# Kernel tuning notes

Measured on AMD Instinct MI355X. Metric: run time of the kernel, lower is better.

## Reference

```python
import jax, jax.numpy as jnp
import numpy as np

N_NODES = 8192
N_EDGES = 262144
IN_DIM = 128
HID = 256


def _sage_conv(x, src, dst, w_l, b_l, w_r, n):
    # PyG SAGEConv: out = lin_l(mean_{j in N(i)} x_j) + lin_r(x_i)
    agg = jax.ops.segment_sum(x[src], dst, num_segments=n)          # [n, d]
    deg = jax.ops.segment_sum(jnp.ones_like(src, dtype=x.dtype), dst, num_segments=n)
    mean = agg / jnp.maximum(deg, 1.0)[:, None]
    return mean @ w_l.T + b_l + x @ w_r.T


def setup_inputs() -> dict:
    key = jax.random.key(0)
    ks = jax.random.split(key, 12)
    s = lambda d: 1.0 / np.sqrt(d)
    x = jax.random.normal(ks[0], (N_NODES, IN_DIM), dtype=jnp.float32)
    edge_index = jax.random.randint(ks[1], (2, N_EDGES), 0, N_NODES, dtype=jnp.int64)
    return {
        "x": x,
        "edge_index": edge_index,
        "wl1": jax.random.uniform(ks[2], (HID, IN_DIM), jnp.float32, -s(IN_DIM), s(IN_DIM)),
        "bl1": jax.random.uniform(ks[3], (HID,), jnp.float32, -s(IN_DIM), s(IN_DIM)),
        "wr1": jax.random.uniform(ks[4], (HID, IN_DIM), jnp.float32, -s(IN_DIM), s(IN_DIM)),
        "wl2": jax.random.uniform(ks[5], (HID, HID), jnp.float32, -s(HID), s(HID)),
        "bl2": jax.random.uniform(ks[6], (HID,), jnp.float32, -s(HID), s(HID)),
        "wr2": jax.random.uniform(ks[7], (HID, HID), jnp.float32, -s(HID), s(HID)),
        "w_out": jax.random.uniform(ks[8], (HID, HID), jnp.float32, -s(HID), s(HID)),
        "b_out": jax.random.uniform(ks[9], (HID,), jnp.float32, -s(HID), s(HID)),
        "w_edge": jax.random.uniform(ks[10], (1, 2 * HID), jnp.float32, -s(2 * HID), s(2 * HID)),
        "b_edge": jax.random.uniform(ks[11], (1,), jnp.float32, -s(2 * HID), s(2 * HID)),
    }


def reference(x, edge_index, wl1, bl1, wr1, wl2, bl2, wr2, w_out, b_out, w_edge, b_edge):
    n = x.shape[0]
    src, dst = edge_index[0], edge_index[1]
    h = jax.nn.relu(_sage_conv(x, src, dst, wl1, bl1, wr1, n))
    h = jax.nn.relu(_sage_conv(h, src, dst, wl2, bl2, wr2, n))
    h = h @ w_out.T + b_out                                          # [n, HID]
    # edge_logits[i, j] = edge_proj(cat(h_i, h_j)) == <w_left, h_i> + <w_right, h_j> + b
    w_left, w_right = w_edge[0, :HID], w_edge[0, HID:]
    li = h @ w_left                                                  # [n]
    lj = h @ w_right                                                 # [n]
    return li[:, None] + lj[None, :] + b_edge[0]                     # [n, n]
```

## Files before the change

### kernel.cpp

```cpp
#include <hip/hip_runtime.h>

#define NN   8192
#define NE   262144
#define IND  128
#define HIDD 256

typedef __bf16 v8bf __attribute__((ext_vector_type(8)));
typedef float  v4f  __attribute__((ext_vector_type(4)));

__device__ __forceinline__ float bf2f(unsigned short u) {
  unsigned int v = ((unsigned int)u) << 16;
  return __builtin_bit_cast(float, v);
}
__device__ __forceinline__ unsigned short f2bf(float f) {
  unsigned int u = __builtin_bit_cast(unsigned int, f);
  u += 0x7FFF + ((u >> 16) & 1);
  return (unsigned short)(u >> 16);
}

__global__ void k_buildW1(const float* __restrict__ wl1,
                          const float* __restrict__ wr1,
                          unsigned short* __restrict__ W1) {
  int t = blockIdx.x * 256 + threadIdx.x;
  int n = t >> 8, k = t & 255;
  float v = (k < 128) ? wl1[n * 128 + k] : wr1[n * 128 + (k - 128)];
  W1[t] = f2bf(v);
}
__global__ void k_buildW2(const float* __restrict__ wl2,
                          const float* __restrict__ wr2,
                          unsigned short* __restrict__ W2) {
  int t = blockIdx.x * 256 + threadIdx.x;
  int n = t >> 9, k = t & 511;
  float v = (k < 256) ? wl2[n * 256 + k] : wr2[n * 256 + (k - 256)];
  W2[t] = f2bf(v);
}
__global__ void k_vlr(const float* __restrict__ w_out,
                      const float* __restrict__ b_out,
                      const float* __restrict__ w_edge,
                      float* __restrict__ vl, float* __restrict__ vr,
                      float* __restrict__ c2) {
  int k = threadIdx.x;
  float al = 0.f, ar = 0.f;
  for (int n = 0; n < 256; n++) {
    float w = w_out[n * 256 + k];
    al += w * w_edge[n];
    ar += w * w_edge[256 + n];
  }
  vl[k] = al; vr[k] = ar;
  __shared__ float red[256];
  red[k] = b_out[k] * w_edge[k];
  __syncthreads();
  for (int s = 128; s > 0; s >>= 1) { if (k < s) red[k] += red[k + s]; __syncthreads(); }
  if (k == 0) c2[0] = red[0];
  __syncthreads();
  red[k] = b_out[k] * w_edge[256 + k];
  __syncthreads();
  for (int s = 128; s > 0; s >>= 1) { if (k < s) red[k] += red[k + s]; __syncthreads(); }
  if (k == 0) c2[1] = red[0];
}

__global__ void k_count(const int* __restrict__ dst, int* __restrict__ counts) {
  int e = blockIdx.x * 256 + threadIdx.x;
  if (e < NE) atomicAdd(&counts[dst[e]], 1);
}
__global__ void k_scan(const int* __restrict__ counts, int* __restrict__ offs,
                       int* __restrict__ curs, float* __restrict__ ideg) {
  __shared__ int sums[256];
  int t = threadIdx.x;
  int base = t * 32;
  int s = 0;
  for (int i = 0; i < 32; i++) s += counts[base + i];
  sums[t] = s;
  __syncthreads();
  for (int off = 1; off < 256; off <<= 1) {
    int v = (t >= off) ? sums[t - off] : 0;
    __syncthreads();
    sums[t] += v;
    __syncthreads();
  }
  int run = (t == 0) ? 0 : sums[t - 1];
  for (int i = 0; i < 32; i++) {
    int c = counts[base + i];
    offs[base + i] = run;
    curs[base + i] = run;
    ideg[base + i] = 1.0f / (float)(c > 0 ? c : 1);
    run += c;
  }
}
__global__ void k_fill(const int* __restrict__ src, const int* __restrict__ dst,
                       int* __restrict__ curs, int* __restrict__ csr) {
  int e = blockIdx.x * 256 + threadIdx.x;
  if (e < NE) {
    int d = dst[e];
    int p = atomicAdd(&curs[d], 1);
    csr[p] = src[e];
  }
}

__global__ void k_copyx(const float* __restrict__ x, unsigned short* __restrict__ A1) {
  int t = blockIdx.x * 256 + threadIdx.x;
  int row = t >> 4, c8 = (t & 15) << 3;
  const float* xp = &x[row * 128 + c8];
  float4 a = *(const float4*)xp;
  float4 b = *(const float4*)(xp + 4);
  unsigned short o[8];
  o[0] = f2bf(a.x); o[1] = f2bf(a.y); o[2] = f2bf(a.z); o[3] = f2bf(a.w);
  o[4] = f2bf(b.x); o[5] = f2bf(b.y); o[6] = f2bf(b.z); o[7] = f2bf(b.w);
  *(uint4*)&A1[row * 256 + 128 + c8] = *(uint4*)o;
}

__global__ void k_gather_f32(const float* __restrict__ feat,
                             unsigned short* __restrict__ outp,
                             const int* __restrict__ offs, const int* __restrict__ counts,
                             const float* __restrict__ ideg, const int* __restrict__ csr) {
  int node = blockIdx.x;
  int t = threadIdx.x;
  int start = offs[node], cnt = counts[node];
  const float* fp = feat + t;
  float acc = 0.f;
  int i = 0;
  for (; i + 4 <= cnt; i += 4) {
    int s0 = csr[start + i], s1 = csr[start + i + 1];
    int s2 = csr[start + i + 2], s3 = csr[start + i + 3];
    acc += fp[(size_t)s0 * IND];
    acc += fp[(size_t)s1 * IND];
    acc += fp[(size_t)s2 * IND];
    acc += fp[(size_t)s3 * IND];
  }
  for (; i < cnt; i++) acc += fp[(size_t)csr[start + i] * IND];
  outp[(size_t)node * 256 + t] = f2bf(acc * ideg[node]);
}

__global__ void k_gather_bf16(const unsigned short* __restrict__ feat, int fstride, int foff,
                              unsigned short* __restrict__ outp, int ostride, int ooff,
                              const int* __restrict__ offs, const int* __restrict__ counts,
                              const float* __restrict__ ideg, const int* __restrict__ csr) {
  int node = blockIdx.x;
  int t = threadIdx.x;
  int start = offs[node], cnt = counts[node];
  const unsigned short* fp = feat + foff + t;
  float acc = 0.f;
  int i = 0;
  for (; i + 4 <= cnt; i += 4) {
    int s0 = csr[start + i], s1 = csr[start + i + 1];
    int s2 = csr[start + i + 2], s3 = csr[start + i + 3];
    acc += bf2f(fp[(size_t)s0 * fstride]);
    acc += bf2f(fp[(size_t)s1 * fstride]);
    acc += bf2f(fp[(size_t)s2 * fstride]);
    acc += bf2f(fp[(size_t)s3 * fstride]);
  }
  for (; i < cnt; i++) acc += bf2f(fp[(size_t)csr[start + i] * fstride]);
  outp[(size_t)node * ostride + ooff + t] = f2bf(acc * ideg[node]);
}

__global__ __launch_bounds__(256) void k_gemm(
    const unsigned short* __restrict__ A, int lda,
    const unsigned short* __restrict__ B,
    const float* __restrict__ bias,
    unsigned short* __restrict__ C, int ldc, int coff, int K) {
  __shared__ __align__(16) unsigned short As[64][40];
  __shared__ __align__(16) unsigned short Bs[64][40];
  int tid = threadIdx.x;
  int bm = blockIdx.x, bn = blockIdx.y;
  int lane = tid & 63, wave = tid >> 6;
  int wm = (wave & 1) * 32, wn = (wave >> 1) * 32;
  int quad = lane >> 4, l16 = lane & 15;
  int srow = tid >> 2, schunk = (tid & 3) * 8;
  const unsigned short* gA = A + (size_t)(bm * 64 + srow) * lda + schunk;
  const unsigned short* gB = B + (size_t)(bn * 64 + srow) * K + schunk;
  v4f acc[2][2];
  for (int mi = 0; mi < 2; mi++)
    for (int ni = 0; ni < 2; ni++)
      acc[mi][ni] = v4f{0.f, 0.f, 0.f, 0.f};
  for (int k0 = 0; k0 < K; k0 += 32) {
    uint4 va = *(const uint4*)(gA + k0);
    uint4 vb = *(const uint4*)(gB + k0);
    __syncthreads();
    *(uint4*)&As[srow][schunk] = va;
    *(uint4*)&Bs[srow][schunk] = vb;
    __syncthreads();
    v8bf a0 = *(v8bf*)&As[wm + l16][quad * 8];
    v8bf a1 = *(v8bf*)&As[wm + 16 + l16][quad * 8];
    v8bf b0 = *(v8bf*)&Bs[wn + l16][quad * 8];
    v8bf b1 = *(v8bf*)&Bs[wn + 16 + l16][quad * 8];
    acc[0][0] = __builtin_amdgcn_mfma_f32_16x16x32_bf16(a0, b0, acc[0][0], 0, 0, 0);
    acc[0][1] = __builtin_amdgcn_mfma_f32_16x16x32_bf16(a0, b1, acc[0][1], 0, 0, 0);
    acc[1][0] = __builtin_amdgcn_mfma_f32_16x16x32_bf16(a1, b0, acc[1][0], 0, 0, 0);
    acc[1][1] = __builtin_amdgcn_mfma_f32_16x16x32_bf16(a1, b1, acc[1][1], 0, 0, 0);
  }
  for (int mi = 0; mi < 2; mi++) {
    for (int ni = 0; ni < 2; ni++) {
      int col = bn * 64 + wn + ni * 16 + l16;
      float bv = bias[col];
      for (int r = 0; r < 4; r++) {
        int row = bm * 64 + wm + mi * 16 + quad * 4 + r;
        float v = acc[mi][ni][r] + bv;
        v = fmaxf(v, 0.f);
        C[(size_t)row * ldc + coff + col] = f2bf(v);
      }
    }
  }
}

__global__ void k_lilj(const unsigned short* __restrict__ H2,
                       const float* __restrict__ vl, const float* __restrict__ vr,
                       const float* __restrict__ c2, const float* __restrict__ b_edge,
                       float* __restrict__ Li, float* __restrict__ Lj) {
  int wave = threadIdx.x >> 6, lane = threadIdx.x & 63;
  int node = blockIdx.x * 4 + wave;
  const unsigned short* h = H2 + (size_t)node * 256;
  float al = 0.f, ar = 0.f;
  for (int k = lane; k < 256; k += 64) {
    float hv = bf2f(h[k]);
    al += hv * vl[k];
    ar += hv * vr[k];
  }
  for (int off = 32; off > 0; off >>= 1) {
    al += __shfl_down(al, off);
    ar += __shfl_down(ar, off);
  }
  if (lane == 0) {
    Li[node] = al + c2[0] + b_edge[0];
    Lj[node] = ar + c2[1];
  }
}

__global__ void k_outer(const float* __restrict__ Li, const float* __restrict__ Lj,
                        float* __restrict__ outp) {
  int t = blockIdx.x * 256 + threadIdx.x;
  int row = t >> 10;
  int jc = (t & 1023) << 3;
  float li = Li[row];
  float4 x0 = *(const float4*)&Lj[jc];
  float4 x1 = *(const float4*)&Lj[jc + 4];
  float4 o0, o1;
  o0.x = li + x0.x; o0.y = li + x0.y; o0.z = li + x0.z; o0.w = li + x0.w;
  o1.x = li + x1.x; o1.y = li + x1.y; o1.z = li + x1.z; o1.w = li + x1.w;
  float* op = &outp[(size_t)row * 8192 + jc];
  *(float4*)op = o0;
  *(float4*)(op + 4) = o1;
}

extern "C" void kernel_launch(void* const* d_in, const int* in_sizes, int n_in,
                              void* d_out, int out_size, void* d_ws, size_t ws_size,
                              hipStream_t stream) {
  const float* x      = (const float*)d_in[0];
  const int*   ei     = (const int*)d_in[1];
  const float* wl1    = (const float*)d_in[2];
  const float* bl1    = (const float*)d_in[3];
  const float* wr1    = (const float*)d_in[4];
  const float* wl2    = (const float*)d_in[5];
  const float* bl2    = (const float*)d_in[6];
  const float* wr2    = (const float*)d_in[7];
  const float* w_out  = (const float*)d_in[8];
  const float* b_out  = (const float*)d_in[9];
  const float* w_edge = (const float*)d_in[10];
  const float* b_edge = (const float*)d_in[11];
  float* outp = (float*)d_out;

  const int* srcp = ei;
  const int* dstp = ei + NE;

  const size_t OFF_A1   = 0;
  const size_t OFF_A2   = OFF_A1 + 4194304;
  const size_t OFF_H2   = OFF_A2 + 8388608;
  const size_t OFF_W1   = OFF_H2 + 4194304;
  const size_t OFF_W2   = OFF_W1 + 131072;
  const size_t OFF_VL   = OFF_W2 + 262144;
  const size_t OFF_VR   = OFF_VL + 1024;
  const size_t OFF_C2   = OFF_VR + 1024;
  const size_t OFF_CNT  = OFF_C2 + 256;
  const size_t OFF_OFFS = OFF_CNT + 32768;
  const size_t OFF_CURS = OFF_OFFS + 32768;
  const size_t OFF_IDEG = OFF_CURS + 32768;
  const size_t OFF_CSR  = OFF_IDEG + 32768;
  const size_t OFF_LI   = OFF_CSR + 1048576;
  const size_t OFF_LJ   = OFF_LI + 32768;
  const size_t TOTAL    = OFF_LJ + 32768;
  if (ws_size < TOTAL) return;

  char* ws = (char*)d_ws;
  unsigned short* A1 = (unsigned short*)(ws + OFF_A1);
  unsigned short* A2 = (unsigned short*)(ws + OFF_A2);
  unsigned short* H2 = (unsigned short*)(ws + OFF_H2);
  unsigned short* W1 = (unsigned short*)(ws + OFF_W1);
  unsigned short* W2 = (unsigned short*)(ws + OFF_W2);
  float* VL   = (float*)(ws + OFF_VL);
  float* VR   = (float*)(ws + OFF_VR);
  float* C2   = (float*)(ws + OFF_C2);
  int*   CNT  = (int*)(ws + OFF_CNT);
  int*   OFFS = (int*)(ws + OFF_OFFS);
  int*   CURS = (int*)(ws + OFF_CURS);
  float* IDEG = (float*)(ws + OFF_IDEG);
  int*   CSR  = (int*)(ws + OFF_CSR);
  float* LI   = (float*)(ws + OFF_LI);
  float* LJ   = (float*)(ws + OFF_LJ);

  hipMemsetAsync(CNT, 0, NN * sizeof(int), stream);

  k_buildW1<<<256, 256, 0, stream>>>(wl1, wr1, W1);
  k_buildW2<<<512, 256, 0, stream>>>(wl2, wr2, W2);
  k_vlr<<<1, 256, 0, stream>>>(w_out, b_out, w_edge, VL, VR, C2);
  k_copyx<<<512, 256, 0, stream>>>(x, A1);

  k_count<<<NE / 256, 256, 0, stream>>>(dstp, CNT);
  k_scan<<<1, 256, 0, stream>>>(CNT, OFFS, CURS, IDEG);
  k_fill<<<NE / 256, 256, 0, stream>>>(srcp, dstp, CURS, CSR);

  k_gather_f32<<<NN, 128, 0, stream>>>(x, A1, OFFS, CNT, IDEG, CSR);
  k_gemm<<<dim3(NN / 64, 4), 256, 0, stream>>>(A1, 256, W1, bl1, A2, 512, 256, 256);

  k_gather_bf16<<<NN, 256, 0, stream>>>(A2, 512, 256, A2, 512, 0, OFFS, CNT, IDEG, CSR);
  k_gemm<<<dim3(NN / 64, 4), 256, 0, stream>>>(A2, 512, W2, bl2, H2, 256, 0, 512);

  k_lilj<<<NN / 4, 256, 0, stream>>>(H2, VL, VR, C2, b_edge, LI, LJ);
  k_outer<<<(NN * 1024) / 256, 256, 0, stream>>>(LI, LJ, outp);
}
```

Before: 425.1 us.

## Fuse prep kernels, wave-per-node vectorized gathers, fuse GEMM2 with logit projection

Merges the weight packing, x conversion, counter zeroing and vl/vr computation into one multi-role launch. Rewrites both neighbour gathers to use one wave per node with vectorized loads and several accumulators. Fuses the second GEMM epilogue with the li/lj dot products via shuffle reductions and atomics, which removes the H2 buffer and the k_lilj pass. The outer-sum kernel now uses nontemporal stores and folds the constants in. The risks are float atomic ordering nondeterminism and contention on the LI/LJ atomics.

```diff
diff --git a/kernel.cpp b/kernel.cpp
--- a/kernel.cpp
+++ b/kernel.cpp
@@ -18,45 +18,66 @@
   return (unsigned short)(u >> 16);
 }
 
-__global__ void k_buildW1(const float* __restrict__ wl1,
-                          const float* __restrict__ wr1,
-                          unsigned short* __restrict__ W1) {
-  int t = blockIdx.x * 256 + threadIdx.x;
-  int n = t >> 8, k = t & 255;
-  float v = (k < 128) ? wl1[n * 128 + k] : wr1[n * 128 + (k - 128)];
-  W1[t] = f2bf(v);
-}
-__global__ void k_buildW2(const float* __restrict__ wl2,
-                          const float* __restrict__ wr2,
-                          unsigned short* __restrict__ W2) {
-  int t = blockIdx.x * 256 + threadIdx.x;
-  int n = t >> 9, k = t & 511;
-  float v = (k < 256) ? wl2[n * 256 + k] : wr2[n * 256 + (k - 256)];
-  W2[t] = f2bf(v);
-}
-__global__ void k_vlr(const float* __restrict__ w_out,
-                      const float* __restrict__ b_out,
-                      const float* __restrict__ w_edge,
-                      float* __restrict__ vl, float* __restrict__ vr,
-                      float* __restrict__ c2) {
-  int k = threadIdx.x;
-  float al = 0.f, ar = 0.f;
-  for (int n = 0; n < 256; n++) {
-    float w = w_out[n * 256 + k];
-    al += w * w_edge[n];
-    ar += w * w_edge[256 + n];
-  }
-  vl[k] = al; vr[k] = ar;
+__global__ void k_prep(const float* __restrict__ wl1, const float* __restrict__ wr1,
+                       const float* __restrict__ wl2, const float* __restrict__ wr2,
+                       const float* __restrict__ x,
+                       const float* __restrict__ w_out, const float* __restrict__ b_out,
+                       const float* __restrict__ w_edge,
+                       unsigned short* __restrict__ W1, unsigned short* __restrict__ W2,
+                       unsigned short* __restrict__ A1,
+                       float* __restrict__ VL, float* __restrict__ VR,
+                       float* __restrict__ C2,
+                       int* __restrict__ CNT,
+                       float* __restrict__ LI, float* __restrict__ LJ) {
   __shared__ float red[256];
-  red[k] = b_out[k] * w_edge[k];
-  __syncthreads();
-  for (int s = 128; s > 0; s >>= 1) { if (k < s) red[k] += red[k + s]; __syncthreads(); }
-  if (k == 0) c2[0] = red[0];
-  __syncthreads();
-  red[k] = b_out[k] * w_edge[256 + k];
-  __syncthreads();
-  for (int s = 128; s > 0; s >>= 1) { if (k < s) red[k] += red[k + s]; __syncthreads(); }
-  if (k == 0) c2[1] = red[0];
+  int b = blockIdx.x, tid = threadIdx.x;
+  if (b < 256) {
+    int t = b * 256 + tid;
+    int n = t >> 8, k = t & 255;
+    float v = (k < 128) ? wl1[n * 128 + k] : wr1[n * 128 + (k - 128)];
+    W1[t] = f2bf(v);
+  } else if (b < 768) {
+    int t = (b - 256) * 256 + tid;
+    int n = t >> 9, k = t & 511;
+    float v = (k < 256) ? wl2[n * 256 + k] : wr2[n * 256 + (k - 256)];
+    W2[t] = f2bf(v);
+  } else if (b < 1280) {
+    int t = (b - 768) * 256 + tid;
+    int row = t >> 4, c8 = (t & 15) << 3;
+    const float* xp = &x[row * 128 + c8];
+    float4 a = *(const float4*)xp;
+    float4 bb = *(const float4*)(xp + 4);
+    unsigned short o[8];
+    o[0] = f2bf(a.x);  o[1] = f2bf(a.y);  o[2] = f2bf(a.z);  o[3] = f2bf(a.w);
+    o[4] = f2bf(bb.x); o[5] = f2bf(bb.y); o[6] = f2bf(bb.z); o[7] = f2bf(bb.w);
+    *(uint4*)&A1[row * 256 + 128 + c8] = *(uint4*)o;
+  } else if (b < 1312) {
+    CNT[(b - 1280) * 256 + tid] = 0;
+  } else if (b < 1344) {
+    int t = (b - 1312) * 256 + tid;
+    LI[t] = 0.f; LJ[t] = 0.f;
+  } else {
+    int k = tid;
+    float al = 0.f, ar = 0.f;
+    for (int n = 0; n < 256; n += 8) {
+#pragma unroll
+      for (int u = 0; u < 8; u++) {
+        float w = w_out[(n + u) * 256 + k];
+        al = fmaf(w, w_edge[n + u], al);
+        ar = fmaf(w, w_edge[256 + n + u], ar);
+      }
+    }
+    VL[k] = al; VR[k] = ar;
+    red[k] = b_out[k] * w_edge[k];
+    __syncthreads();
+    for (int s = 128; s > 0; s >>= 1) { if (k < s) red[k] += red[k + s]; __syncthreads(); }
+    if (k == 0) C2[0] = red[0];
+    __syncthreads();
+    red[k] = b_out[k] * w_edge[256 + k];
+    __syncthreads();
+    for (int s = 128; s > 0; s >>= 1) { if (k < s) red[k] += red[k + s]; __syncthreads(); }
+    if (k == 0) C2[1] = red[0];
+  }
 }
 
 __global__ void k_count(const int* __restrict__ dst, int* __restrict__ counts) {
@@ -68,8 +89,12 @@
   __shared__ int sums[256];
   int t = threadIdx.x;
   int base = t * 32;
+  int c[32];
+#pragma unroll
+  for (int i = 0; i < 32; i += 4) *(int4*)&c[i] = *(const int4*)&counts[base + i];
   int s = 0;
-  for (int i = 0; i < 32; i++) s += counts[base + i];
+#pragma unroll
+  for (int i = 0; i < 32; i++) s += c[i];
   sums[t] = s;
   __syncthreads();
   for (int off = 1; off < 256; off <<= 1) {
@@ -79,12 +104,12 @@
     __syncthreads();
   }
   int run = (t == 0) ? 0 : sums[t - 1];
+#pragma unroll
   for (int i = 0; i < 32; i++) {
-    int c = counts[base + i];
     offs[base + i] = run;
     curs[base + i] = run;
-    ideg[base + i] = 1.0f / (float)(c > 0 ? c : 1);
-    run += c;
+    ideg[base + i] = 1.0f / (float)(c[i] > 0 ? c[i] : 1);
+    run += c[i];
   }
 }
 __global__ void k_fill(const int* __restrict__ src, const int* __restrict__ dst,
@@ -97,60 +122,72 @@
   }
 }
 
-__global__ void k_copyx(const float* __restrict__ x, unsigned short* __restrict__ A1) {
-  int t = blockIdx.x * 256 + threadIdx.x;
-  int row = t >> 4, c8 = (t & 15) << 3;
-  const float* xp = &x[row * 128 + c8];
-  float4 a = *(const float4*)xp;
-  float4 b = *(const float4*)(xp + 4);
-  unsigned short o[8];
-  o[0] = f2bf(a.x); o[1] = f2bf(a.y); o[2] = f2bf(a.z); o[3] = f2bf(a.w);
-  o[4] = f2bf(b.x); o[5] = f2bf(b.y); o[6] = f2bf(b.z); o[7] = f2bf(b.w);
-  *(uint4*)&A1[row * 256 + 128 + c8] = *(uint4*)o;
-}
-
-__global__ void k_gather_f32(const float* __restrict__ feat,
-                             unsigned short* __restrict__ outp,
-                             const int* __restrict__ offs, const int* __restrict__ counts,
-                             const float* __restrict__ ideg, const int* __restrict__ csr) {
-  int node = blockIdx.x;
-  int t = threadIdx.x;
+__global__ void k_gather1(const float* __restrict__ x, unsigned short* __restrict__ A1,
+                          const int* __restrict__ offs, const int* __restrict__ counts,
+                          const float* __restrict__ ideg, const int* __restrict__ csr) {
+  int lane = threadIdx.x & 63;
+  int node = blockIdx.x * 4 + (threadIdx.x >> 6);
   int start = offs[node], cnt = counts[node];
-  const float* fp = feat + t;
-  float acc = 0.f;
+  const float2* fp = (const float2*)x + lane;
+  float ax0 = 0.f, ay0 = 0.f, ax1 = 0.f, ay1 = 0.f;
+  int i = 0;
+  for (; i + 8 <= cnt; i += 8) {
+    int s0 = csr[start + i + 0], s1 = csr[start + i + 1];
+    int s2 = csr[start + i + 2], s3 = csr[start + i + 3];
+    int s4 = csr[start + i + 4], s5 = csr[start + i + 5];
+    int s6 = csr[start + i + 6], s7 = csr[start + i + 7];
+    float2 v0 = fp[(size_t)s0 * 64], v1 = fp[(size_t)s1 * 64];
+    float2 v2 = fp[(size_t)s2 * 64], v3 = fp[(size_t)s3 * 64];
+    float2 v4 = fp[(size_t)s4 * 64], v5 = fp[(size_t)s5 * 64];
+    float2 v6 = fp[(size_t)s6 * 64], v7 = fp[(size_t)s7 * 64];
+    ax0 += v0.x; ay0 += v0.y; ax0 += v1.x; ay0 += v1.y;
+    ax0 += v2.x; ay0 += v2.y; ax0 += v3.x; ay0 += v3.y;
+    ax1 += v4.x; ay1 += v4.y; ax1 += v5.x; ay1 += v5.y;
+    ax1 += v6.x; ay1 += v6.y; ax1 += v7.x; ay1 += v7.y;
+  }
+  for (; i < cnt; i++) {
+    float2 v = fp[(size_t)csr[start + i] * 64];
+    ax0 += v.x; ay0 += v.y;
+  }
+  float sc = ideg[node];
+  float mx = (ax0 + ax1) * sc, my = (ay0 + ay1) * sc;
+  unsigned int o = (unsigned int)f2bf(mx) | ((unsigned int)f2bf(my) << 16);
+  *(unsigned int*)&A1[(size_t)node * 256 + lane * 2] = o;
+}
+
+__global__ void k_gather2(const unsigned short* __restrict__ A2,
+                          unsigned short* __restrict__ A2w,
+                          const int* __restrict__ offs, const int* __restrict__ counts,
+                          const float* __restrict__ ideg, const int* __restrict__ csr) {
+  int lane = threadIdx.x & 63;
+  int node = blockIdx.x * 4 + (threadIdx.x >> 6);
+  int start = offs[node], cnt = counts[node];
+  const unsigned short* fp = A2 + 256 + lane * 4;
+  float a0 = 0.f, a1 = 0.f, a2 = 0.f, a3 = 0.f;
+#define ACC4(v) { a0 += bf2f((unsigned short)((v).x));        \
+                  a1 += bf2f((unsigned short)((v).x >> 16));  \
+                  a2 += bf2f((unsigned short)((v).y));        \
+                  a3 += bf2f((unsigned short)((v).y >> 16)); }
   int i = 0;
   for (; i + 4 <= cnt; i += 4) {
-    int s0 = csr[start + i], s1 = csr[start + i + 1];
+    int s0 = csr[start + i + 0], s1 = csr[start + i + 1];
     int s2 = csr[start + i + 2], s3 = csr[start + i + 3];
-    acc += fp[(size_t)s0 * IND];
-    acc += fp[(size_t)s1 * IND];
-    acc += fp[(size_t)s2 * IND];
-    acc += fp[(size_t)s3 * IND];
-  }
-  for (; i < cnt; i++) acc += fp[(size_t)csr[start + i] * IND];
-  outp[(size_t)node * 256 + t] = f2bf(acc * ideg[node]);
-}
-
-__global__ void k_gather_bf16(const unsigned short* __restrict__ feat, int fstride, int foff,
-                              unsigned short* __restrict__ outp, int ostride, int ooff,
-                              const int* __restrict__ offs, const int* __restrict__ counts,
-                              const float* __restrict__ ideg, const int* __restrict__ csr) {
-  int node = blockIdx.x;
-  int t = threadIdx.x;
-  int start = offs[node], cnt = counts[node];
-  const unsigned short* fp = feat + foff + t;
-  float acc = 0.f;
-  int i = 0;
-  for (; i + 4 <= cnt; i += 4) {
-    int s0 = csr[start + i], s1 = csr[start + i + 1];
-    int s2 = csr[start + i + 2], s3 = csr[start + i + 3];
-    acc += bf2f(fp[(size_t)s0 * fstride]);
-    acc += bf2f(fp[(size_t)s1 * fstride]);
-    acc += bf2f(fp[(size_t)s2 * fstride]);
-    acc += bf2f(fp[(size_t)s3 * fstride]);
-  }
-  for (; i < cnt; i++) acc += bf2f(fp[(size_t)csr[start + i] * fstride]);
-  outp[(size_t)node * ostride + ooff + t] = f2bf(acc * ideg[node]);
+    uint2 v0 = *(const uint2*)&fp[(size_t)s0 * 512];
+    uint2 v1 = *(const uint2*)&fp[(size_t)s1 * 512];
+    uint2 v2 = *(const uint2*)&fp[(size_t)s2 * 512];
+    uint2 v3 = *(const uint2*)&fp[(size_t)s3 * 512];
+    ACC4(v0); ACC4(v1); ACC4(v2); ACC4(v3);
+  }
+  for (; i < cnt; i++) {
+    uint2 v = *(const uint2*)&fp[(size_t)csr[start + i] * 512];
+    ACC4(v);
+  }
+#undef ACC4
+  float sc = ideg[node];
+  unsigned int lo = (unsigned int)f2bf(a0 * sc) | ((unsigned int)f2bf(a1 * sc) << 16);
+  unsigned int hi = (unsigned int)f2bf(a2 * sc) | ((unsigned int)f2bf(a3 * sc) << 16);
+  uint2 o; o.x = lo; o.y = hi;
+  *(uint2*)&A2w[(size_t)node * 512 + lane * 4] = o;
 }
 
 __global__ __launch_bounds__(256) void k_gemm(
@@ -202,43 +239,93 @@
   }
 }
 
-__global__ void k_lilj(const unsigned short* __restrict__ H2,
-                       const float* __restrict__ vl, const float* __restrict__ vr,
-                       const float* __restrict__ c2, const float* __restrict__ b_edge,
-                       float* __restrict__ Li, float* __restrict__ Lj) {
-  int wave = threadIdx.x >> 6, lane = threadIdx.x & 63;
-  int node = blockIdx.x * 4 + wave;
-  const unsigned short* h = H2 + (size_t)node * 256;
-  float al = 0.f, ar = 0.f;
-  for (int k = lane; k < 256; k += 64) {
-    float hv = bf2f(h[k]);
-    al += hv * vl[k];
-    ar += hv * vr[k];
-  }
-  for (int off = 32; off > 0; off >>= 1) {
-    al += __shfl_down(al, off);
-    ar += __shfl_down(ar, off);
-  }
-  if (lane == 0) {
-    Li[node] = al + c2[0] + b_edge[0];
-    Lj[node] = ar + c2[1];
+__global__ __launch_bounds__(256) void k_gemm2_lilj(
+    const unsigned short* __restrict__ A,
+    const unsigned short* __restrict__ B,
+    const float* __restrict__ bias,
+    const float* __restrict__ VL, const float* __restrict__ VR,
+    float* __restrict__ LI, float* __restrict__ LJ) {
+  __shared__ __align__(16) unsigned short As[64][40];
+  __shared__ __align__(16) unsigned short Bs[64][40];
+  int tid = threadIdx.x;
+  int bm = blockIdx.x, bn = blockIdx.y;
+  int lane = tid & 63, wave = tid >> 6;
+  int wm = (wave & 1) * 32, wn = (wave >> 1) * 32;
+  int quad = lane >> 4, l16 = lane & 15;
+  int srow = tid >> 2, schunk = (tid & 3) * 8;
+  const unsigned short* gA = A + (size_t)(bm * 64 + srow) * 512 + schunk;
+  const unsigned short* gB = B + (size_t)(bn * 64 + srow) * 512 + schunk;
+  v4f acc[2][2];
+  for (int mi = 0; mi < 2; mi++)
+    for (int ni = 0; ni < 2; ni++)
+      acc[mi][ni] = v4f{0.f, 0.f, 0.f, 0.f};
+  for (int k0 = 0; k0 < 512; k0 += 32) {
+    uint4 va = *(const uint4*)(gA + k0);
+    uint4 vb = *(const uint4*)(gB + k0);
+    __syncthreads();
+    *(uint4*)&As[srow][schunk] = va;
+    *(uint4*)&Bs[srow][schunk] = vb;
+    __syncthreads();
+    v8bf a0 = *(v8bf*)&As[wm + l16][quad * 8];
+    v8bf a1 = *(v8bf*)&As[wm + 16 + l16][quad * 8];
+    v8bf b0 = *(v8bf*)&Bs[wn + l16][quad * 8];
+    v8bf b1 = *(v8bf*)&Bs[wn + 16 + l16][quad * 8];
+    acc[0][0] = __builtin_amdgcn_mfma_f32_16x16x32_bf16(a0, b0, acc[0][0], 0, 0, 0);
+    acc[0][1] = __builtin_amdgcn_mfma_f32_16x16x32_bf16(a0, b1, acc[0][1], 0, 0, 0);
+    acc[1][0] = __builtin_amdgcn_mfma_f32_16x16x32_bf16(a1, b0, acc[1][0], 0, 0, 0);
+    acc[1][1] = __builtin_amdgcn_mfma_f32_16x16x32_bf16(a1, b1, acc[1][1], 0, 0, 0);
+  }
+  int colb = bn * 64 + wn + l16;
+  float vl0 = VL[colb], vl1 = VL[colb + 16];
+  float vr0 = VR[colb], vr1 = VR[colb + 16];
+  float bv0 = bias[colb], bv1 = bias[colb + 16];
+  float pli[8], plj[8];
+#pragma unroll
+  for (int mi = 0; mi < 2; mi++) {
+#pragma unroll
+    for (int r = 0; r < 4; r++) {
+      float v0 = fmaxf(acc[mi][0][r] + bv0, 0.f);
+      float v1 = fmaxf(acc[mi][1][r] + bv1, 0.f);
+      pli[mi * 4 + r] = v0 * vl0 + v1 * vl1;
+      plj[mi * 4 + r] = v0 * vr0 + v1 * vr1;
+    }
+  }
+#pragma unroll
+  for (int off = 1; off < 16; off <<= 1) {
+#pragma unroll
+    for (int idx = 0; idx < 8; idx++) {
+      pli[idx] += __shfl_xor(pli[idx], off);
+      plj[idx] += __shfl_xor(plj[idx], off);
+    }
+  }
+  if (l16 == 0) {
+#pragma unroll
+    for (int mi = 0; mi < 2; mi++) {
+#pragma unroll
+      for (int r = 0; r < 4; r++) {
+        int row = bm * 64 + wm + mi * 16 + quad * 4 + r;
+        atomicAdd(&LI[row], pli[mi * 4 + r]);
+        atomicAdd(&LJ[row], plj[mi * 4 + r]);
+      }
+    }
   }
 }
 
 __global__ void k_outer(const float* __restrict__ Li, const float* __restrict__ Lj,
+                        const float* __restrict__ C2, const float* __restrict__ b_edge,
                         float* __restrict__ outp) {
   int t = blockIdx.x * 256 + threadIdx.x;
   int row = t >> 10;
   int jc = (t & 1023) << 3;
-  float li = Li[row];
-  float4 x0 = *(const float4*)&Lj[jc];
-  float4 x1 = *(const float4*)&Lj[jc + 4];
-  float4 o0, o1;
-  o0.x = li + x0.x; o0.y = li + x0.y; o0.z = li + x0.z; o0.w = li + x0.w;
-  o1.x = li + x1.x; o1.y = li + x1.y; o1.z = li + x1.z; o1.w = li + x1.w;
+  float cst = C2[0] + C2[1] + b_edge[0];
+  float li = Li[row] + cst;
+  v4f x0 = *(const v4f*)&Lj[jc];
+  v4f x1 = *(const v4f*)&Lj[jc + 4];
+  v4f o0 = x0 + li;
+  v4f o1 = x1 + li;
   float* op = &outp[(size_t)row * 8192 + jc];
-  *(float4*)op = o0;
-  *(float4*)(op + 4) = o1;
+  __builtin_nontemporal_store(o0, (v4f*)op);
+  __builtin_nontemporal_store(o1, (v4f*)(op + 4));
 }
 
 extern "C" void kernel_launch(void* const* d_in, const int* in_sizes, int n_in,
@@ -263,8 +350,7 @@
 
   const size_t OFF_A1   = 0;
   const size_t OFF_A2   = OFF_A1 + 4194304;
-  const size_t OFF_H2   = OFF_A2 + 8388608;
-  const size_t OFF_W1   = OFF_H2 + 4194304;
+  const size_t OFF_W1   = OFF_A2 + 8388608;
   const size_t OFF_W2   = OFF_W1 + 131072;
   const size_t OFF_VL   = OFF_W2 + 262144;
   const size_t OFF_VR   = OFF_VL + 1024;
@@ -282,7 +368,6 @@
   char* ws = (char*)d_ws;
   unsigned short* A1 = (unsigned short*)(ws + OFF_A1);
   unsigned short* A2 = (unsigned short*)(ws + OFF_A2);
-  unsigned short* H2 = (unsigned short*)(ws + OFF_H2);
   unsigned short* W1 = (unsigned short*)(ws + OFF_W1);
   unsigned short* W2 = (unsigned short*)(ws + OFF_W2);
   float* VL   = (float*)(ws + OFF_VL);
@@ -296,23 +381,18 @@
   float* LI   = (float*)(ws + OFF_LI);
   float* LJ   = (float*)(ws + OFF_LJ);
 
-  hipMemsetAsync(CNT, 0, NN * sizeof(int), stream);
-
-  k_buildW1<<<256, 256, 0, stream>>>(wl1, wr1, W1);
-  k_buildW2<<<512, 256, 0, stream>>>(wl2, wr2, W2);
-  k_vlr<<<1, 256, 0, stream>>>(w_out, b_out, w_edge, VL, VR, C2);
-  k_copyx<<<512, 256, 0, stream>>>(x, A1);
+  k_prep<<<1345, 256, 0, stream>>>(wl1, wr1, wl2, wr2, x, w_out, b_out, w_edge,
+                                   W1, W2, A1, VL, VR, C2, CNT, LI, LJ);
 
   k_count<<<NE / 256, 256, 0, stream>>>(dstp, CNT);
   k_scan<<<1, 256, 0, stream>>>(CNT, OFFS, CURS, IDEG);
   k_fill<<<NE / 256, 256, 0, stream>>>(srcp, dstp, CURS, CSR);
 
-  k_gather_f32<<<NN, 128, 0, stream>>>(x, A1, OFFS, CNT, IDEG, CSR);
+  k_gather1<<<NN / 4, 256, 0, stream>>>(x, A1, OFFS, CNT, IDEG, CSR);
   k_gemm<<<dim3(NN / 64, 4), 256, 0, stream>>>(A1, 256, W1, bl1, A2, 512, 256, 256);
 
-  k_gather_bf16<<<NN, 256, 0, stream>>>(A2, 512, 256, A2, 512, 0, OFFS, CNT, IDEG, CSR);
-  k_gemm<<<dim3(NN / 64, 4), 256, 0, stream>>>(A2, 512, W2, bl2, H2, 256, 0, 512);
-
-  k_lilj<<<NN / 4, 256, 0, stream>>>(H2, VL, VR, C2, b_edge, LI, LJ);
-  k_outer<<<(NN * 1024) / 256, 256, 0, stream>>>(LI, LJ, outp);
-}
+  k_gather2<<<NN / 4, 256, 0, stream>>>(A2, A2, OFFS, CNT, IDEG, CSR);
+  k_gemm2_lilj<<<dim3(NN / 64, 4), 256, 0, stream>>>(A2, W2, bl2, VL, VR, LI, LJ);
+
+  k_outer<<<(NN * 1024) / 256, 256, 0, stream>>>(LI, LJ, C2, b_edge, outp);
+}
```

Result: slower. 454.3 us (+6.9%).
